# Performance work log

Hardware: AMD Instinct MI355X
Metric: run time of the kernel (lower is better)

## Reference

```python
import jax, jax.numpy as jnp
import numpy as np

KERNEL_MUL = 2.0
KERNEL_NUM = 5


def _mmd(src, tar):
    """Multi-bandwidth Gaussian-kernel MMD, matching torch MMDLoss.mmd."""
    B = src.shape[0]
    total = jnp.concatenate([src, tar], axis=0)          # [2B, D]
    sq = jnp.sum(total * total, axis=1)                  # [2B]
    # ||a-b||^2 = ||a||^2 + ||b||^2 - 2 a.b  (GEMM form of the broadcast subtract)
    dist = sq[:, None] + sq[None, :] - 2.0 * (total @ total.T)  # [2B, 2B]
    n = 2 * B
    # torch uses L2_distance.data -> bandwidth is detached from the graph
    bandwidth = jax.lax.stop_gradient(jnp.sum(dist)) / (n * n - n)
    bandwidth = bandwidth / (KERNEL_MUL ** (KERNEL_NUM // 2))
    kernel = sum(jnp.exp(-dist / (bandwidth * KERNEL_MUL ** k)) for k in range(KERNEL_NUM))
    XX = kernel[:B, :B]
    YY = kernel[B:, B:]
    XY = kernel[:B, B:]
    YX = kernel[B:, :B]
    return jnp.mean(XX + YY - XY - YX)


def setup_inputs() -> dict:
    key = jax.random.key(0)
    k1, k2, k3 = jax.random.split(key, 3)
    B, IN, OUT, L = 4096, 512, 256, 2
    x = jax.random.normal(k1, (B, IN), dtype=jnp.float32)
    W_aux = jax.random.normal(k2, (L, IN), dtype=jnp.float32) * (1.0 / np.sqrt(IN))
    b_aux = jnp.zeros((L,), dtype=jnp.float32)
    W = jax.random.normal(k3, (L, OUT, IN), dtype=jnp.float32) * (1.0 / np.sqrt(IN))
    b = jnp.zeros((L, OUT), dtype=jnp.float32)
    return {"x": x, "W_aux": W_aux, "b_aux": b_aux, "W": W, "b": b}


def reference(x, W_aux, b_aux, W, b):
    L = W.shape[0]
    gates = jax.nn.softmax(x @ W_aux.T + b_aux, axis=-1)      # [B, L]
    outs = jnp.einsum('bi,loi->blo', x, W) + b                # [B, L, out]
    combine = jnp.einsum('bl,blo->bo', gates, outs)           # soft-gated combine
    loss = 0.0
    for i in range(L):
        for j in range(i + 1, L):
            loss = loss + _mmd(outs[:, i, :], outs[:, j, :])
    inter_mmd = loss * 2.0 / (L * L - L)
    return combine, -inter_mmd
```

## Files before the change

kernel.cpp:

```cpp
#include <hip/hip_runtime.h>
#include <stdint.h>
#include <math.h>

typedef __attribute__((ext_vector_type(8))) __bf16 bf16x8;
typedef __attribute__((ext_vector_type(4))) __bf16 bf16x4;
typedef __attribute__((ext_vector_type(4))) float f32x4;

__device__ __forceinline__ void gload_lds16(const __bf16* g, __bf16* l) {
  __builtin_amdgcn_global_load_lds(
      (const __attribute__((address_space(1))) unsigned int*)g,
      (__attribute__((address_space(3))) unsigned int*)l,
      16, 0, 0);
}

__global__ __launch_bounds__(256) void k_gates(const float* __restrict__ x,
                                               const float* __restrict__ Waux,
                                               const float* __restrict__ baux,
                                               float* __restrict__ gates) {
  const int wave = threadIdx.x >> 6;
  const int lane = threadIdx.x & 63;
  const int row = blockIdx.x * 4 + wave;
  const float4* xr = (const float4*)(x + (size_t)row * 512);
  const float4* w0 = (const float4*)(Waux);
  const float4* w1 = (const float4*)(Waux + 512);
  float p0 = 0.f, p1 = 0.f;
  for (int c = lane; c < 128; c += 64) {
    float4 xv = xr[c];
    float4 a = w0[c], b = w1[c];
    p0 += xv.x * a.x + xv.y * a.y + xv.z * a.z + xv.w * a.w;
    p1 += xv.x * b.x + xv.y * b.y + xv.z * b.z + xv.w * b.w;
  }
  for (int off = 32; off; off >>= 1) {
    p0 += __shfl_down(p0, off, 64);
    p1 += __shfl_down(p1, off, 64);
  }
  if (lane == 0) {
    p0 += baux[0]; p1 += baux[1];
    float m = fmaxf(p0, p1);
    float e0 = __expf(p0 - m), e1 = __expf(p1 - m);
    float inv = 1.f / (e0 + e1);
    gates[row * 2 + 0] = e0 * inv;
    gates[row * 2 + 1] = e1 * inv;
  }
}

__global__ __launch_bounds__(256) void k_outs(const float* __restrict__ x,
                                              const float* __restrict__ W,
                                              const float* __restrict__ bias,
                                              __bf16* __restrict__ totalbf) {
  __shared__ __bf16 As[64][64];
  __shared__ __bf16 Bs[64][64];
  const int bj = blockIdx.x;
  const int bi = blockIdx.y;
  const int t = threadIdx.x;
  const int wid = t >> 6, lane = t & 63;
  const int wr = wid >> 1, wc = wid & 1;
  const int n16 = lane & 15, q = lane >> 4;
  const int sx = (n16 & 7) << 3;
  const int erow = t >> 4;
  const int c4 = (t & 15) << 2;

  f32x4 acc[2][2];
  f32x4 zero = {0.f, 0.f, 0.f, 0.f};
  for (int i = 0; i < 2; ++i)
    for (int j = 0; j < 2; ++j) acc[i][j] = zero;

  const int arow0 = bi * 64, brow0 = bj * 64;

  float4 ra[4], rb[4];
#pragma unroll
  for (int p = 0; p < 4; ++p) {
    int row = p * 16 + erow;
    ra[p] = *(const float4*)(x + (size_t)(arow0 + row) * 512 + c4);
    rb[p] = *(const float4*)(W + (size_t)(brow0 + row) * 512 + c4);
  }

  for (int kc = 0; kc < 512; kc += 64) {
#pragma unroll
    for (int p = 0; p < 4; ++p) {
      int row = p * 16 + erow;
      int col = c4 ^ ((row & 7) << 3);
      float4 va = ra[p];
      bf16x4 ba = {(__bf16)va.x, (__bf16)va.y, (__bf16)va.z, (__bf16)va.w};
      *(bf16x4*)&As[row][col] = ba;
      float4 vb = rb[p];
      bf16x4 bb = {(__bf16)vb.x, (__bf16)vb.y, (__bf16)vb.z, (__bf16)vb.w};
      *(bf16x4*)&Bs[row][col] = bb;
    }
    if (kc < 448) {
#pragma unroll
      for (int p = 0; p < 4; ++p) {
        int row = p * 16 + erow;
        ra[p] = *(const float4*)(x + (size_t)(arow0 + row) * 512 + kc + 64 + c4);
        rb[p] = *(const float4*)(W + (size_t)(brow0 + row) * 512 + kc + 64 + c4);
      }
    }
    __syncthreads();
#pragma unroll
    for (int ks = 0; ks < 2; ++ks) {
      bf16x8 af[2], bfr[2];
#pragma unroll
      for (int f = 0; f < 2; ++f) {
        af[f]  = *(const bf16x8*)&As[wr * 32 + f * 16 + n16][(ks * 32 + q * 8) ^ sx];
        bfr[f] = *(const bf16x8*)&Bs[wc * 32 + f * 16 + n16][(ks * 32 + q * 8) ^ sx];
      }
      for (int fr = 0; fr < 2; ++fr)
        for (int fc = 0; fc < 2; ++fc)
          acc[fr][fc] = __builtin_amdgcn_mfma_f32_16x16x32_bf16(af[fr], bfr[fc], acc[fr][fc], 0, 0, 0);
    }
    __syncthreads();
  }

  for (int fc = 0; fc < 2; ++fc) {
    int n_g = bj * 64 + wc * 32 + fc * 16 + n16;
    float bv = bias[n_g];
    int l = n_g >> 8, o = n_g & 255;
    for (int fr = 0; fr < 2; ++fr) {
      for (int r = 0; r < 4; ++r) {
        int m_g = bi * 64 + wr * 32 + fr * 16 + q * 4 + r;
        float v = acc[fr][fc][r] + bv;
        totalbf[(size_t)(l * 4096 + m_g) * 256 + o] = (__bf16)v;
      }
    }
  }
}

__global__ __launch_bounds__(256) void k_sq(const __bf16* __restrict__ tot,
                                            float* __restrict__ sq,
                                            float* __restrict__ colsum) {
  __shared__ float lcol[4][256];
  const int t = threadIdx.x;
  const int wave = t >> 6, lane = t & 63;
  float c0 = 0.f, c1 = 0.f, c2 = 0.f, c3 = 0.f;
  for (int it = 0; it < 8; ++it) {
    int row = blockIdx.x * 32 + wave * 8 + it;
    bf16x4 v = *(const bf16x4*)(tot + (size_t)row * 256 + lane * 4);
    float f0 = v[0], f1 = v[1], f2 = v[2], f3 = v[3];
    float s = f0 * f0 + f1 * f1 + f2 * f2 + f3 * f3;
    for (int off = 32; off; off >>= 1) s += __shfl_down(s, off, 64);
    if (lane == 0) sq[row] = s;
    c0 += f0; c1 += f1; c2 += f2; c3 += f3;
  }
  lcol[wave][lane * 4 + 0] = c0;
  lcol[wave][lane * 4 + 1] = c1;
  lcol[wave][lane * 4 + 2] = c2;
  lcol[wave][lane * 4 + 3] = c3;
  __syncthreads();
  float s2 = lcol[0][t] + lcol[1][t] + lcol[2][t] + lcol[3][t];
  atomicAdd(&colsum[t], s2);
}

__global__ __launch_bounds__(256) void k_bw(const float* __restrict__ sq,
                                            const float* __restrict__ colsum,
                                            float* __restrict__ scal) {
  __shared__ float red[256];
  const int t = threadIdx.x;
  float s = 0.f;
  for (int i = t; i < 8192; i += 256) s += sq[i];
  red[t] = s;
  __syncthreads();
  for (int off = 128; off; off >>= 1) { if (t < off) red[t] += red[t + off]; __syncthreads(); }
  float sumsq = red[0];
  __syncthreads();
  float c = colsum[t];
  red[t] = c * c;
  __syncthreads();
  for (int off = 128; off; off >>= 1) { if (t < off) red[t] += red[t + off]; __syncthreads(); }
  if (t == 0) {
    double sumdist = 2.0 * 8192.0 * (double)sumsq - 2.0 * (double)red[0];
    double bw = sumdist / (8192.0 * 8192.0 - 8192.0) / 4.0;
    scal[1] = (float)(1.4426950408889634 / (bw * 16.0));
    scal[2] = (float)bw;
  }
}

__global__ __launch_bounds__(256) void k_combine(const __bf16* __restrict__ tot,
                                                 const float* __restrict__ gates,
                                                 float* __restrict__ out) {
  int idx = blockIdx.x * 256 + threadIdx.x;
  int b = idx >> 6;
  int oc = (idx & 63) * 4;
  float g0 = gates[b * 2], g1 = gates[b * 2 + 1];
  bf16x4 v0 = *(const bf16x4*)(tot + (size_t)b * 256 + oc);
  bf16x4 v1 = *(const bf16x4*)(tot + (size_t)(4096 + b) * 256 + oc);
  float4 r;
  r.x = g0 * (float)v0[0] + g1 * (float)v1[0];
  r.y = g0 * (float)v0[1] + g1 * (float)v1[1];
  r.z = g0 * (float)v0[2] + g1 * (float)v1[2];
  r.w = g0 * (float)v0[3] + g1 * (float)v1[3];
  *(float4*)(out + (size_t)b * 256 + oc) = r;
}

__global__ __launch_bounds__(256) void k_gram(const __bf16* __restrict__ tot,
                                              const float* __restrict__ sq,
                                              const float* __restrict__ scal,
                                              float* __restrict__ Ssum) {
  const int b = blockIdx.x;
  const int nid = (b & 7) * 260 + (b >> 3);
  int ti = (int)((129.0 - sqrt(129.0 * 129.0 - 8.0 * (double)nid)) * 0.5);
  while (64 * ti - ti * (ti - 1) / 2 > nid) --ti;
  while (64 * (ti + 1) - (ti + 1) * ti / 2 <= nid) ++ti;
  const int tj = ti + (nid - (64 * ti - ti * (ti - 1) / 2));

  __shared__ __bf16 As[2][128][64];
  __shared__ __bf16 Bs[2][128][64];
  __shared__ float sqi[128], sqj[128];
  __shared__ float wred[4];
  const int t = threadIdx.x;
  const int wid = t >> 6, lane = t & 63;
  const int wr = wid >> 1, wc = wid & 1;
  const int n16 = lane & 15, q = lane >> 4;
  const int sx = (n16 & 7) << 3;
  const int lr = lane >> 3;
  const int ls = lane & 7;

  if (t < 128) sqi[t] = sq[ti * 128 + t];
  else         sqj[t - 128] = sq[tj * 128 + (t - 128)];

  f32x4 acc[4][4];
  f32x4 zero = {0.f, 0.f, 0.f, 0.f};
  for (int i = 0; i < 4; ++i)
    for (int j = 0; j < 4; ++j) acc[i][j] = zero;

  const __bf16* gA = tot + (size_t)(ti * 128 + wid * 32 + lr) * 256 + ((ls ^ lr) << 3);
  const __bf16* gB = tot + (size_t)(tj * 128 + wid * 32 + lr) * 256 + ((ls ^ lr) << 3);

#pragma unroll
  for (int p = 0; p < 4; ++p) {
    gload_lds16(gA + p * 8 * 256, &As[0][wid * 32 + p * 8][0]);
    gload_lds16(gB + p * 8 * 256, &Bs[0][wid * 32 + p * 8][0]);
  }
  __syncthreads();

  int buf = 0;
  for (int it = 0; it < 4; ++it) {
    if (it < 3) {
      const int kc = (it + 1) * 64;
#pragma unroll
      for (int p = 0; p < 4; ++p) {
        gload_lds16(gA + p * 8 * 256 + kc, &As[buf ^ 1][wid * 32 + p * 8][0]);
        gload_lds16(gB + p * 8 * 256 + kc, &Bs[buf ^ 1][wid * 32 + p * 8][0]);
      }
    }
#pragma unroll
    for (int ks = 0; ks < 2; ++ks) {
      bf16x8 af[4], bfr[4];
#pragma unroll
      for (int f = 0; f < 4; ++f) {
        af[f]  = *(const bf16x8*)&As[buf][wr * 64 + f * 16 + n16][(ks * 32 + q * 8) ^ sx];
        bfr[f] = *(const bf16x8*)&Bs[buf][wc * 64 + f * 16 + n16][(ks * 32 + q * 8) ^ sx];
      }
      for (int fr = 0; fr < 4; ++fr)
        for (int fc = 0; fc < 4; ++fc)
          acc[fr][fc] = __builtin_amdgcn_mfma_f32_16x16x32_bf16(af[fr], bfr[fc], acc[fr][fc], 0, 0, 0);
    }
    __syncthreads();
    buf ^= 1;
  }

  const float g = scal[1];
  float lsum = 0.f;
  for (int fr = 0; fr < 4; ++fr) {
    for (int r = 0; r < 4; ++r) {
      float si = sqi[wr * 64 + fr * 16 + q * 4 + r];
      for (int fc = 0; fc < 4; ++fc) {
        float sj = sqj[wc * 64 + fc * 16 + n16];
        float dist = si + sj - 2.f * acc[fr][fc][r];
        float e = exp2f(-dist * g);
        float e2 = e * e, e4 = e2 * e2, e8 = e4 * e4, e16 = e8 * e8;
        lsum += e + e2 + e4 + e8 + e16;
      }
    }
  }
  for (int off = 32; off; off >>= 1) lsum += __shfl_down(lsum, off, 64);
  if (lane == 0) wred[wid] = lsum;
  __syncthreads();
  if (t == 0) {
    float blocksum = wred[0] + wred[1] + wred[2] + wred[3];
    float sgn = ((ti < 32) == (tj < 32)) ? 1.f : -1.f;
    float wgt = (ti == tj) ? sgn : 2.f * sgn;
    atomicAdd(Ssum, wgt * blocksum);
  }
}

__global__ void k_final(const float* __restrict__ scal, float* __restrict__ out) {
  out[1048576] = -(scal[0] / 16777216.0f);
}

extern "C" void kernel_launch(void* const* d_in, const int* in_sizes, int n_in,
                              void* d_out, int out_size, void* d_ws, size_t ws_size,
                              hipStream_t stream) {
  const float* x    = (const float*)d_in[0];
  const float* Waux = (const float*)d_in[1];
  const float* baux = (const float*)d_in[2];
  const float* W    = (const float*)d_in[3];
  const float* bias = (const float*)d_in[4];
  float* out = (float*)d_out;

  char* ws = (char*)d_ws;
  __bf16* totalbf = (__bf16*)ws;
  float* sq      = (float*)(ws + 4194304);
  float* colsum  = (float*)(ws + 4227072);
  float* scal    = (float*)(ws + 4228096);
  float* gates   = (float*)(ws + 4228160);

  hipMemsetAsync(ws + 4227072, 0, 1024 + 64, stream);

  k_gates<<<1024, 256, 0, stream>>>(x, Waux, baux, gates);
  k_outs<<<dim3(8, 64), 256, 0, stream>>>(x, W, bias, totalbf);
  k_sq<<<256, 256, 0, stream>>>(totalbf, sq, colsum);
  k_bw<<<1, 256, 0, stream>>>(sq, colsum, scal);
  k_combine<<<1024, 256, 0, stream>>>(totalbf, gates, out);
  k_gram<<<2080, 256, 0, stream>>>(totalbf, sq, scal, scal);
  k_final<<<1, 1, 0, stream>>>(scal, out);
}
```

Baseline: 151.4 us.

## Fuse combine into sq kernel, single-buffer gram tiles, fold final into gram

Merges the gated-combine step into the row-norm/column-sum kernel so the two expert rows are read once per output row, and removes the separate combine launch. The Gram kernel drops LDS double buffering in favour of single-buffered tiles with s_setprio around the MFMAs and a 4-blocks-per-SM launch bound. It also prescales the squared norms by the bandwidth factor so each exponent is one FMA. The final loss is written by the last-finishing block via an atomic counter, removing the k_final launch. Single buffering trades load/compute overlap for occupancy, and the counter relies on the memset that clears the workspace.

New measurement: 172.9 us. 14.2% more time.

```diff
diff --git a/kernel.cpp b/kernel.cpp
--- a/kernel.cpp
+++ b/kernel.cpp
@@ -125,21 +125,36 @@
   }
 }
 
-__global__ __launch_bounds__(256) void k_sq(const __bf16* __restrict__ tot,
-                                            float* __restrict__ sq,
-                                            float* __restrict__ colsum) {
+__global__ __launch_bounds__(256) void k_sqc(const __bf16* __restrict__ tot,
+                                             const float* __restrict__ gates,
+                                             float* __restrict__ sq,
+                                             float* __restrict__ colsum,
+                                             float* __restrict__ out) {
   __shared__ float lcol[4][256];
   const int t = threadIdx.x;
   const int wave = t >> 6, lane = t & 63;
   float c0 = 0.f, c1 = 0.f, c2 = 0.f, c3 = 0.f;
   for (int it = 0; it < 8; ++it) {
-    int row = blockIdx.x * 32 + wave * 8 + it;
-    bf16x4 v = *(const bf16x4*)(tot + (size_t)row * 256 + lane * 4);
-    float f0 = v[0], f1 = v[1], f2 = v[2], f3 = v[3];
-    float s = f0 * f0 + f1 * f1 + f2 * f2 + f3 * f3;
-    for (int off = 32; off; off >>= 1) s += __shfl_down(s, off, 64);
-    if (lane == 0) sq[row] = s;
-    c0 += f0; c1 += f1; c2 += f2; c3 += f3;
+    int m = blockIdx.x * 32 + wave * 8 + it;
+    bf16x4 v0 = *(const bf16x4*)(tot + (size_t)m * 256 + lane * 4);
+    bf16x4 v1 = *(const bf16x4*)(tot + (size_t)(4096 + m) * 256 + lane * 4);
+    float f00 = v0[0], f01 = v0[1], f02 = v0[2], f03 = v0[3];
+    float f10 = v1[0], f11 = v1[1], f12 = v1[2], f13 = v1[3];
+    float s0 = f00 * f00 + f01 * f01 + f02 * f02 + f03 * f03;
+    float s1 = f10 * f10 + f11 * f11 + f12 * f12 + f13 * f13;
+    for (int off = 32; off; off >>= 1) {
+      s0 += __shfl_down(s0, off, 64);
+      s1 += __shfl_down(s1, off, 64);
+    }
+    if (lane == 0) { sq[m] = s0; sq[4096 + m] = s1; }
+    c0 += f00 + f10; c1 += f01 + f11; c2 += f02 + f12; c3 += f03 + f13;
+    float2 gv = *(const float2*)(gates + m * 2);
+    float4 r;
+    r.x = gv.x * f00 + gv.y * f10;
+    r.y = gv.x * f01 + gv.y * f11;
+    r.z = gv.x * f02 + gv.y * f12;
+    r.w = gv.x * f03 + gv.y * f13;
+    *(float4*)(out + (size_t)m * 256 + lane * 4) = r;
   }
   lcol[wave][lane * 4 + 0] = c0;
   lcol[wave][lane * 4 + 1] = c1;
@@ -174,27 +189,11 @@
   }
 }
 
-__global__ __launch_bounds__(256) void k_combine(const __bf16* __restrict__ tot,
-                                                 const float* __restrict__ gates,
+__global__ __launch_bounds__(256, 4) void k_gram(const __bf16* __restrict__ tot,
+                                                 const float* __restrict__ sq,
+                                                 const float* __restrict__ scal,
+                                                 float* __restrict__ Ssum,
                                                  float* __restrict__ out) {
-  int idx = blockIdx.x * 256 + threadIdx.x;
-  int b = idx >> 6;
-  int oc = (idx & 63) * 4;
-  float g0 = gates[b * 2], g1 = gates[b * 2 + 1];
-  bf16x4 v0 = *(const bf16x4*)(tot + (size_t)b * 256 + oc);
-  bf16x4 v1 = *(const bf16x4*)(tot + (size_t)(4096 + b) * 256 + oc);
-  float4 r;
-  r.x = g0 * (float)v0[0] + g1 * (float)v1[0];
-  r.y = g0 * (float)v0[1] + g1 * (float)v1[1];
-  r.z = g0 * (float)v0[2] + g1 * (float)v1[2];
-  r.w = g0 * (float)v0[3] + g1 * (float)v1[3];
-  *(float4*)(out + (size_t)b * 256 + oc) = r;
-}
-
-__global__ __launch_bounds__(256) void k_gram(const __bf16* __restrict__ tot,
-                                              const float* __restrict__ sq,
-                                              const float* __restrict__ scal,
-                                              float* __restrict__ Ssum) {
   const int b = blockIdx.x;
   const int nid = (b & 7) * 260 + (b >> 3);
   int ti = (int)((129.0 - sqrt(129.0 * 129.0 - 8.0 * (double)nid)) * 0.5);
@@ -202,8 +201,8 @@
   while (64 * (ti + 1) - (ti + 1) * ti / 2 <= nid) ++ti;
   const int tj = ti + (nid - (64 * ti - ti * (ti - 1) / 2));
 
-  __shared__ __bf16 As[2][128][64];
-  __shared__ __bf16 Bs[2][128][64];
+  __shared__ __bf16 As[128][64];
+  __shared__ __bf16 Bs[128][64];
   __shared__ float sqi[128], sqj[128];
   __shared__ float wred[4];
   const int t = threadIdx.x;
@@ -214,8 +213,9 @@
   const int lr = lane >> 3;
   const int ls = lane & 7;
 
-  if (t < 128) sqi[t] = sq[ti * 128 + t];
-  else         sqj[t - 128] = sq[tj * 128 + (t - 128)];
+  const float g = scal[1];
+  if (t < 128) sqi[t] = sq[ti * 128 + t] * g;
+  else         sqj[t - 128] = sq[tj * 128 + (t - 128)] * g;
 
   f32x4 acc[4][4];
   f32x4 zero = {0.f, 0.f, 0.f, 0.f};
@@ -225,50 +225,42 @@
   const __bf16* gA = tot + (size_t)(ti * 128 + wid * 32 + lr) * 256 + ((ls ^ lr) << 3);
   const __bf16* gB = tot + (size_t)(tj * 128 + wid * 32 + lr) * 256 + ((ls ^ lr) << 3);
 
-#pragma unroll
-  for (int p = 0; p < 4; ++p) {
-    gload_lds16(gA + p * 8 * 256, &As[0][wid * 32 + p * 8][0]);
-    gload_lds16(gB + p * 8 * 256, &Bs[0][wid * 32 + p * 8][0]);
-  }
-  __syncthreads();
-
-  int buf = 0;
   for (int it = 0; it < 4; ++it) {
-    if (it < 3) {
-      const int kc = (it + 1) * 64;
-#pragma unroll
-      for (int p = 0; p < 4; ++p) {
-        gload_lds16(gA + p * 8 * 256 + kc, &As[buf ^ 1][wid * 32 + p * 8][0]);
-        gload_lds16(gB + p * 8 * 256 + kc, &Bs[buf ^ 1][wid * 32 + p * 8][0]);
-      }
-    }
+    const int kc = it * 64;
+#pragma unroll
+    for (int p = 0; p < 4; ++p) {
+      gload_lds16(gA + p * 8 * 256 + kc, &As[wid * 32 + p * 8][0]);
+      gload_lds16(gB + p * 8 * 256 + kc, &Bs[wid * 32 + p * 8][0]);
+    }
+    __syncthreads();
+    __builtin_amdgcn_s_setprio(1);
 #pragma unroll
     for (int ks = 0; ks < 2; ++ks) {
       bf16x8 af[4], bfr[4];
 #pragma unroll
       for (int f = 0; f < 4; ++f) {
-        af[f]  = *(const bf16x8*)&As[buf][wr * 64 + f * 16 + n16][(ks * 32 + q * 8) ^ sx];
-        bfr[f] = *(const bf16x8*)&Bs[buf][wc * 64 + f * 16 + n16][(ks * 32 + q * 8) ^ sx];
+        af[f]  = *(const bf16x8*)&As[wr * 64 + f * 16 + n16][(ks * 32 + q * 8) ^ sx];
+        bfr[f] = *(const bf16x8*)&Bs[wc * 64 + f * 16 + n16][(ks * 32 + q * 8) ^ sx];
       }
       for (int fr = 0; fr < 4; ++fr)
         for (int fc = 0; fc < 4; ++fc)
           acc[fr][fc] = __builtin_amdgcn_mfma_f32_16x16x32_bf16(af[fr], bfr[fc], acc[fr][fc], 0, 0, 0);
     }
+    __builtin_amdgcn_s_setprio(0);
     __syncthreads();
-    buf ^= 1;
-  }
-
-  const float g = scal[1];
+  }
+
+  const float twog = 2.f * g;
   float lsum = 0.f;
   for (int fr = 0; fr < 4; ++fr) {
     for (int r = 0; r < 4; ++r) {
-      float si = sqi[wr * 64 + fr * 16 + q * 4 + r];
+      float gsi = sqi[wr * 64 + fr * 16 + q * 4 + r];
       for (int fc = 0; fc < 4; ++fc) {
-        float sj = sqj[wc * 64 + fc * 16 + n16];
-        float dist = si + sj - 2.f * acc[fr][fc][r];
-        float e = exp2f(-dist * g);
-        float e2 = e * e, e4 = e2 * e2, e8 = e4 * e4, e16 = e8 * e8;
-        lsum += e + e2 + e4 + e8 + e16;
+        float gsj = sqj[wc * 64 + fc * 16 + n16];
+        float u = exp2f(fmaf(twog, acc[fr][fc][r], -(gsi + gsj)));
+        float u2 = u * u, u4 = u2 * u2, u8 = u4 * u4;
+        float s1 = fmaf(u8, u8, u8);
+        lsum += (u + u2) + (u4 + s1);
       }
     }
   }
@@ -280,11 +272,14 @@
     float sgn = ((ti < 32) == (tj < 32)) ? 1.f : -1.f;
     float wgt = (ti == tj) ? sgn : 2.f * sgn;
     atomicAdd(Ssum, wgt * blocksum);
-  }
-}
-
-__global__ void k_final(const float* __restrict__ scal, float* __restrict__ out) {
-  out[1048576] = -(scal[0] / 16777216.0f);
+    __threadfence();
+    unsigned int* cnt = (unsigned int*)(Ssum + 3);
+    unsigned int c = atomicAdd(cnt, 1u);
+    if (c == 2079u) {
+      float totS = atomicAdd(Ssum, 0.0f);
+      out[1048576] = -(totS / 16777216.0f);
+    }
+  }
 }
 
 extern "C" void kernel_launch(void* const* d_in, const int* in_sizes, int n_in,
@@ -308,9 +303,7 @@
 
   k_gates<<<1024, 256, 0, stream>>>(x, Waux, baux, gates);
   k_outs<<<dim3(8, 64), 256, 0, stream>>>(x, W, bias, totalbf);
-  k_sq<<<256, 256, 0, stream>>>(totalbf, sq, colsum);
+  k_sqc<<<128, 256, 0, stream>>>(totalbf, gates, sq, colsum, out);
   k_bw<<<1, 256, 0, stream>>>(sq, colsum, scal);
-  k_combine<<<1024, 256, 0, stream>>>(totalbf, gates, out);
-  k_gram<<<2080, 256, 0, stream>>>(totalbf, sq, scal, scal);
-  k_final<<<1, 1, 0, stream>>>(scal, out);
-}
+  k_gram<<<2080, 256, 0, stream>>>(totalbf, sq, scal, scal, out);
+}
```
